# Kernel tuning notes

Measured on AMD Instinct MI355X. Metric: run time of the kernel, lower is better.

Reference implementation:

```python
import math
import jax, jax.numpy as jnp
import numpy as np

EPS = 1e-8


def setup_inputs() -> dict:
    key = jax.random.key(0)
    k0, k1, k2, k3 = jax.random.split(key, 4)
    B, C_IN, C_OUT, H, W, K, S = 8, 256, 256, 128, 128, 3, 512
    return {
        "input": jax.random.normal(k0, (B, C_IN, H, W), dtype=jnp.float32),
        "style": jax.random.normal(k1, (B, S), dtype=jnp.float32),
        # learned params
        "weight": jax.random.normal(k2, (1, C_OUT, C_IN, K, K), dtype=jnp.float32),
        "mod_weight": jax.random.normal(k3, (C_IN, S), dtype=jnp.float32),
        "mod_bias": jnp.ones((C_IN,), dtype=jnp.float32),  # bias_init=1
    }


def reference(input, style, weight, mod_weight, mod_bias):
    B, C_in, H, W = input.shape
    _, C_out, _, K, _ = weight.shape
    S = mod_weight.shape[1]

    # EqualLinear modulation: F.linear(style, w * (1/sqrt(S))) + bias (lr_mul=1)
    lin_scale = 1.0 / math.sqrt(S)
    s = style @ (mod_weight.T * lin_scale) + mod_bias  # [B, C_in]

    # per-sample weight modulation
    conv_scale = 1.0 / math.sqrt(C_in * K * K)  # fan_in scale
    w = conv_scale * weight * s[:, None, :, None, None]  # [B, C_out, C_in, K, K]

    # demodulation
    demod = jax.lax.rsqrt(jnp.sum(w * w, axis=(2, 3, 4)) + EPS)  # [B, C_out]
    w = w * demod[:, :, None, None, None]

    # groups=batch conv2d with padding=k//2 (same spatial size)
    pad = K // 2

    def conv_one(x, wk):  # x: [C_in, H, W], wk: [C_out, C_in, K, K]
        y = jax.lax.conv_general_dilated(
            x[None], wk, window_strides=(1, 1),
            padding=[(pad, pad), (pad, pad)],
            dimension_numbers=("NCHW", "OIHW", "NCHW"))
        return y[0]

    return jax.vmap(conv_one)(input, w)  # [B, C_out, H, W]
```

## Files before the change

### kernel.cpp

```cpp
#include <hip/hip_runtime.h>
#include <hip/hip_bf16.h>

typedef __attribute__((ext_vector_type(8))) short short8;
typedef __attribute__((ext_vector_type(4))) float floatx4;
typedef __attribute__((ext_vector_type(4))) unsigned uint4v;

#define B_ 8
#define C_IN 256
#define C_OUT 256
#define H_ 128
#define W_ 128
#define S_ 512
#define HW_ (H_*W_)
#define LIN_SCALE 0.04419417382415922f
#define CONV_SCALE 0.02083333333333333f
#define EPS_ 1e-8f

#define XPH 130
#define XPW 136
#define TTH 8
#define TTW 32
#define PH2 10
#define PW2 34
#define NPIX2 (PH2*PW2)
#define BUFSZ 24576
#define ABUFSZ 8192
#define ABASE_LDS 49152
#define NKB 72
#define NTHR 256

__device__ __forceinline__ unsigned short f2bf(float f) {
  unsigned u = __builtin_bit_cast(unsigned, f);
  u = (u + 0x7fffu + ((u >> 16) & 1u)) >> 16;
  return (unsigned short)u;
}
__device__ __forceinline__ unsigned pack2(float a, float b) {
  return (unsigned)f2bf(a) | ((unsigned)f2bf(b) << 16);
}
__device__ __forceinline__ void gload16(const void* g, void* l) {
  __builtin_amdgcn_global_load_lds(
      (const __attribute__((address_space(1))) unsigned*)g,
      (__attribute__((address_space(3))) unsigned*)l, 16, 0, 0);
}

__global__ void k_style(const float* __restrict__ style, const float* __restrict__ mw,
                        const float* __restrict__ mb, float* __restrict__ s) {
  __shared__ float sty[S_];
  const int b = blockIdx.x;
  for (int i = threadIdx.x; i < S_; i += 256) sty[i] = style[b*S_ + i];
  __syncthreads();
  const int ci = threadIdx.x;
  const float* wr = mw + (size_t)ci*S_;
  float acc = 0.f;
  for (int i = 0; i < S_; ++i) acc += sty[i] * wr[i];
  s[b*C_IN + ci] = acc * LIN_SCALE + mb[ci];
}

__global__ void k_demod(const float* __restrict__ weight, const float* __restrict__ s,
                        float* __restrict__ demod) {
  const int b = blockIdx.x >> 8, co = blockIdx.x & 255;
  const int l = threadIdx.x;
  const float* wrow = weight + (size_t)co*C_IN*9;
  const float* sb = s + b*C_IN;
  float acc = 0.f;
  for (int idx = l; idx < C_IN*9; idx += 64) {
    float wv = wrow[idx] * sb[idx/9];
    acc += wv*wv;
  }
#pragma unroll
  for (int off = 32; off; off >>= 1) acc += __shfl_down(acc, off, 64);
  if (l == 0) demod[blockIdx.x] = rsqrtf(acc * (CONV_SCALE*CONV_SCALE) + EPS_);
}

__global__ void k_pack(const float* __restrict__ weight, const float* __restrict__ s,
                       const float* __restrict__ demod, unsigned short* __restrict__ frag) {
  const int bid = blockIdx.x;
  const int mt = bid & 15;
  const int kb = (bid >> 4) % NKB;
  const int b  = bid / (NKB*16);
  const int l = threadIdx.x;
  const int co = mt*16 + (l & 15);
  const int chunk = kb / 9, r = kb % 9;
  const float dm = demod[b*C_OUT + co] * CONV_SCALE;
  const float* sb = s + b*C_IN;
  unsigned v[4];
#pragma unroll
  for (int jj = 0; jj < 4; ++jj) {
    int ci0 = chunk*32 + (l >> 4)*8 + jj*2;
    unsigned lo = f2bf(weight[((size_t)co*C_IN + ci0    )*9 + r] * sb[ci0    ] * dm);
    unsigned hi = f2bf(weight[((size_t)co*C_IN + ci0 + 1)*9 + r] * sb[ci0 + 1] * dm);
    v[jj] = lo | (hi << 16);
  }
  unsigned* dst = (unsigned*)(frag + (size_t)bid*512 + l*8);
  dst[0] = v[0]; dst[1] = v[1]; dst[2] = v[2]; dst[3] = v[3];
}

__global__ void k_border(unsigned short* __restrict__ xp) {
  const int plane = blockIdx.x;
  unsigned short* base = xp + (size_t)plane*XPH*XPW*32;
  const uint4v z = {0u,0u,0u,0u};
  for (int i = threadIdx.x; i < 516; i += 256) {
    int hh, ww;
    if (i < 260) { hh = (i < 130) ? 0 : 129; ww = i % 130; }
    else { int j = i - 260; ww = (j < 128) ? 0 : 129; hh = 1 + (j & 127); }
    uint4v* p = (uint4v*)(base + ((size_t)hh*XPW + ww)*32);
    p[0] = z; p[1] = z; p[2] = z; p[3] = z;
  }
}

__global__ void k_xpose(const float* __restrict__ x, unsigned short* __restrict__ xp) {
  __shared__ __align__(16) unsigned lds32[64*128];
  const int bid = blockIdx.x;
  const int half = bid & 1, h = (bid >> 1) & 127, b = bid >> 8;
  const int w0 = half*64;
  const int t = threadIdx.x;
  const float* xr = x + (size_t)b*C_IN*HW_ + (size_t)h*W_ + w0;
#pragma unroll
  for (int j = 0; j < 8; ++j) {
    int cp = j*16 + (t >> 4);
    int ci = cp*2;
    const float* p0 = xr + (size_t)ci*HW_ + (t & 15)*4;
    floatx4 f0 = *(const floatx4*)p0;
    floatx4 f1 = *(const floatx4*)(p0 + HW_);
    int g = cp >> 2, slot = cp & 3;
#pragma unroll
    for (int k = 0; k < 4; ++k) {
      int px = (t & 15)*4 + k;
      lds32[px*128 + ((g ^ ((px >> 2) & 7)) << 2) + slot] = pack2(f0[k], f1[k]);
    }
  }
  __syncthreads();
#pragma unroll
  for (int i = 0; i < 8; ++i) {
    int item = i*256 + t;
    int px = item >> 5, g = item & 31;
    int c = (item >> 2) & 7, sub = item & 3;
    int gs = g ^ ((px >> 2) & 7);
    uint4v v = *(const uint4v*)&lds32[px*128 + (gs << 2)];
    unsigned short* dst = xp +
        (((size_t)(b*8 + c)*XPH + (h + 1))*XPW + (w0 + 1 + px))*32 + sub*8;
    *(uint4v*)dst = v;
  }
}

__launch_bounds__(NTHR, 2)
__global__ void k_conv(const unsigned short* __restrict__ xpad,
                       const unsigned short* __restrict__ frag,
                       float* __restrict__ out) {
  __shared__ __align__(16) unsigned char sm[2*BUFSZ + 4*ABUFSZ];
  const int work = (blockIdx.x & 7)*128 + (blockIdx.x >> 3);
  const int ct = work & 1;
  const int w2 = work >> 1;
  const int sx = w2 & 3, sy = (w2 >> 2) & 15, b = w2 >> 6;
  const int h0 = sy*TTH, w0 = sx*TTW;
  const int tid = threadIdx.x;
  const int lane = tid & 63, wv = tid >> 6;
  const int wm = wv >> 1, wn = wv & 1;
  const int sl = lane >> 4, c15 = lane & 15, wn8 = wn*8;
  const int b8 = b*8;

  floatx4 acc[4][8];
#pragma unroll
  for (int m = 0; m < 4; ++m)
#pragma unroll
    for (int n = 0; n < 8; ++n) acc[m][n] = floatx4{0.f, 0.f, 0.f, 0.f};

  int srcoff[6];
#pragma unroll
  for (int p = 0; p < 6; ++p) {
    int item = p*256 + tid;
    int px = item >> 2, q8s = item & 3;
    if (px > NPIX2 - 1) px = NPIX2 - 1;
    int ph = px / PW2, pw = px - ph*PW2;
    int q8 = q8s ^ ((px >> 1) & 3);
    srcoff[p] = (ph*XPW + pw)*32 + q8*8;
  }
  const unsigned short* abase = frag + ((size_t)b*NKB*16 + ct*8)*512 + (size_t)tid*8;
  const unsigned char* aRd = sm + ABASE_LDS + wm*4096 + lane*16;

  short8 Ar[4], Br[8];

  auto readRegs = [&](int slot, int bbase, int tap) __attribute__((always_inline)) {
    const int dh = tap/3, dw = tap%3;
#pragma unroll
    for (int m = 0; m < 4; ++m)
      Ar[m] = *(const short8*)(aRd + slot*8192 + m*1024);
#pragma unroll
    for (int n = 0; n < 8; ++n) {
      int nt = wn8 + n;
      int pix = ((nt >> 1) + dh)*PW2 + ((nt & 1)*16 + c15 + dw);
      int addr = pix*64 + ((sl ^ ((pix >> 1) & 3)) << 4);
      Br[n] = *(const short8*)(sm + bbase + addr);
    }
  };
  auto mfmaStep = [&]() __attribute__((always_inline)) {
    __builtin_amdgcn_s_setprio(1);
#pragma unroll
    for (int n = 0; n < 8; ++n) {
      acc[0][n] = __builtin_amdgcn_mfma_f32_16x16x32_bf16(Ar[0], Br[n], acc[0][n], 0, 0, 0);
      acc[1][n] = __builtin_amdgcn_mfma_f32_16x16x32_bf16(Ar[1], Br[n], acc[1][n], 0, 0, 0);
      acc[2][n] = __builtin_amdgcn_mfma_f32_16x16x32_bf16(Ar[2], Br[n], acc[2][n], 0, 0, 0);
      acc[3][n] = __builtin_amdgcn_mfma_f32_16x16x32_bf16(Ar[3], Br[n], acc[3][n], 0, 0, 0);
    }
    __builtin_amdgcn_s_setprio(0);
  };

#define SBAR0 __builtin_amdgcn_sched_barrier(0)
#define WAITB(NLIT) do { SBAR0; \
    asm volatile("s_waitcnt vmcnt(" NLIT ")" ::: "memory"); \
    __builtin_amdgcn_s_barrier(); SBAR0; } while (0)

#define STEP(J, R, NLIT) do { \
    WAITB(NLIT); \
    { int kbs = c9 + (R) + 3; if (kbs > NKB-1) kbs = NKB-1; \
      const unsigned short* asrc = abase + (size_t)kbs*8192; \
      unsigned char* adst = sm + ABASE_LDS + ((((J)+(R)+3)&3)*8192) + tid*16; \
      gload16(asrc, adst); gload16(asrc + 2048, adst + 4096); } \
    if ((R) < 6) \
      gload16(xc + srcoff[R], sm + ((((J)+1)&1)*BUFSZ) + ((R)*256 + tid)*16); \
    mfmaStep(); \
    readRegs(((J)+(R)+1)&3, \
             ((R)==8) ? ((((J)+1)&1)*BUFSZ) : (((J)&1)*BUFSZ), \
             ((R)==8) ? 0 : (R)+1); \
  } while (0)

#define CHUNK(J) do { \
    const int c = cc*4 + (J); const int c9 = c*9; \
    const int cn = (c < 7) ? c + 1 : 7; \
    const unsigned short* xc = xpad + (((size_t)(b8 + cn)*XPH + h0)*XPW + w0)*32; \
    STEP(J,0,"2"); STEP(J,1,"3"); STEP(J,2,"3"); \
    STEP(J,3,"3"); STEP(J,4,"3"); STEP(J,5,"3"); \
    STEP(J,6,"3"); STEP(J,7,"2"); STEP(J,8,"2"); \
  } while (0)

  {
    const unsigned short* xc0 = xpad + (((size_t)b8*XPH + h0)*XPW + w0)*32;
#pragma unroll
    for (int p = 0; p < 6; ++p)
      gload16(xc0 + srcoff[p], sm + (p*256 + tid)*16);
#pragma unroll
    for (int s5 = 0; s5 < 3; ++s5) {
      const unsigned short* asrc = abase + (size_t)s5*8192;
      unsigned char* adst = sm + ABASE_LDS + s5*8192 + tid*16;
      gload16(asrc, adst); gload16(asrc + 2048, adst + 4096);
    }
    SBAR0;
    asm volatile("s_waitcnt vmcnt(0)" ::: "memory");
    __builtin_amdgcn_s_barrier();
    SBAR0;
    readRegs(0, 0, 0);
  }

#pragma unroll 1
  for (int cc = 0; cc < 2; ++cc) {
    CHUNK(0); CHUNK(1); CHUNK(2); CHUNK(3);
  }
#undef CHUNK
#undef STEP
#undef WAITB
#undef SBAR0

  float* ob = out + ((size_t)b*C_OUT + ct*128)*HW_;
  const int tw = lane & 15, rg = lane >> 4;
#pragma unroll
  for (int m = 0; m < 4; ++m) {
#pragma unroll
    for (int n = 0; n < 8; ++n) {
      int co = (wm*4 + m)*16 + rg*4;
      int nt = wn8 + n;
      int h = h0 + (nt >> 1);
      int w = w0 + (nt & 1)*16 + tw;
      float* p = ob + (size_t)co*HW_ + (size_t)h*W_ + w;
#pragma unroll
      for (int i = 0; i < 4; ++i) p[i*HW_] = acc[m][n][i];
    }
  }
}

extern "C" void kernel_launch(void* const* d_in, const int* in_sizes, int n_in,
                              void* d_out, int out_size, void* d_ws, size_t ws_size,
                              hipStream_t stream) {
  const float* x      = (const float*)d_in[0];
  const float* style  = (const float*)d_in[1];
  const float* weight = (const float*)d_in[2];
  const float* mod_w  = (const float*)d_in[3];
  const float* mod_b  = (const float*)d_in[4];
  float* out = (float*)d_out;
  char* ws = (char*)d_ws;

  float* s     = (float*)ws;
  float* demod = (float*)(ws + 8192);
  unsigned short* frag = (unsigned short*)(ws + 16384);
  unsigned short* xpad = (unsigned short*)(ws + (16u<<20));

  k_style<<<B_, 256, 0, stream>>>(style, mod_w, mod_b, s);
  k_demod<<<B_*C_OUT, 64, 0, stream>>>(weight, s, demod);
  k_pack<<<B_*NKB*16, 64, 0, stream>>>(weight, s, demod, frag);
  k_border<<<B_*8, 256, 0, stream>>>(xpad);
  k_xpose<<<B_*H_*2, 256, 0, stream>>>(x, xpad);
  k_conv<<<B_*2*16*4, NTHR, 0, stream>>>(xpad, frag, out);
}
```

Measured before the change: 211.6 us.

## Fuse border zeroing into transpose, batch k_pack taps, relax conv vmcnt waits

k_pack now handles all nine kernel taps per block, reading each contiguous 9-float weight row once instead of doing strided per-tap loads, and it launches a ninth as many blocks. The separate k_border launch is removed: k_xpose now zeroes the left/right padding columns for its row and the top/bottom rows when h==0. The vmcnt wait counts in the conv pipeline are loosened from 3 to 4 for the middle steps, allowing more loads in flight. This is meant to cut launch overhead and weight-packing traffic, and to overlap more memory latency in the conv. It risks a hazard if the looser waits let an MFMA read LDS data that has not arrived yet.

```diff
diff --git a/kernel.cpp b/kernel.cpp
--- a/kernel.cpp
+++ b/kernel.cpp
@@ -76,35 +76,29 @@
                        const float* __restrict__ demod, unsigned short* __restrict__ frag) {
   const int bid = blockIdx.x;
   const int mt = bid & 15;
-  const int kb = (bid >> 4) % NKB;
-  const int b  = bid / (NKB*16);
+  const int chunk = (bid >> 4) & 7;
+  const int b  = bid >> 7;
   const int l = threadIdx.x;
   const int co = mt*16 + (l & 15);
-  const int chunk = kb / 9, r = kb % 9;
   const float dm = demod[b*C_OUT + co] * CONV_SCALE;
   const float* sb = s + b*C_IN;
-  unsigned v[4];
+  unsigned v[9][4];
 #pragma unroll
   for (int jj = 0; jj < 4; ++jj) {
     int ci0 = chunk*32 + (l >> 4)*8 + jj*2;
-    unsigned lo = f2bf(weight[((size_t)co*C_IN + ci0    )*9 + r] * sb[ci0    ] * dm);
-    unsigned hi = f2bf(weight[((size_t)co*C_IN + ci0 + 1)*9 + r] * sb[ci0 + 1] * dm);
-    v[jj] = lo | (hi << 16);
-  }
-  unsigned* dst = (unsigned*)(frag + (size_t)bid*512 + l*8);
-  dst[0] = v[0]; dst[1] = v[1]; dst[2] = v[2]; dst[3] = v[3];
-}
-
-__global__ void k_border(unsigned short* __restrict__ xp) {
-  const int plane = blockIdx.x;
-  unsigned short* base = xp + (size_t)plane*XPH*XPW*32;
-  const uint4v z = {0u,0u,0u,0u};
-  for (int i = threadIdx.x; i < 516; i += 256) {
-    int hh, ww;
-    if (i < 260) { hh = (i < 130) ? 0 : 129; ww = i % 130; }
-    else { int j = i - 260; ww = (j < 128) ? 0 : 129; hh = 1 + (j & 127); }
-    uint4v* p = (uint4v*)(base + ((size_t)hh*XPW + ww)*32);
-    p[0] = z; p[1] = z; p[2] = z; p[3] = z;
+    float w0[9], w1[9];
+    __builtin_memcpy(w0, weight + ((size_t)co*C_IN + ci0    )*9, 36);
+    __builtin_memcpy(w1, weight + ((size_t)co*C_IN + ci0 + 1)*9, 36);
+    float s0 = sb[ci0] * dm, s1 = sb[ci0 + 1] * dm;
+#pragma unroll
+    for (int r = 0; r < 9; ++r)
+      v[r][jj] = pack2(w0[r]*s0, w1[r]*s1);
+  }
+#pragma unroll
+  for (int r = 0; r < 9; ++r) {
+    unsigned* dst = (unsigned*)(frag +
+        ((size_t)((b*NKB + chunk*9 + r)*16 + mt))*512 + l*8);
+    dst[0] = v[r][0]; dst[1] = v[r][1]; dst[2] = v[r][2]; dst[3] = v[r][3];
   }
 }
 
@@ -114,6 +108,23 @@
   const int half = bid & 1, h = (bid >> 1) & 127, b = bid >> 8;
   const int w0 = half*64;
   const int t = threadIdx.x;
+  const uint4v z = {0u,0u,0u,0u};
+  if (t < 32) {
+    int chunk = t >> 2, part = t & 3;
+    unsigned short* p = xp +
+        (((size_t)(b*8 + chunk)*XPH + (h + 1))*XPW + half*129)*32 + part*8;
+    *(uint4v*)p = z;
+  }
+  if (h == 0) {
+    for (int i = t; i < 65*2*8*4; i += 256) {
+      int part = i & 3, cell = i >> 2;
+      int wwi = cell % 65; int rest = cell / 65;
+      int rowsel = rest & 1, chunk = rest >> 1;
+      unsigned short* p = xp +
+          (((size_t)(b*8 + chunk)*XPH + rowsel*129)*XPW + (half*65 + wwi))*32 + part*8;
+      *(uint4v*)p = z;
+    }
+  }
   const float* xr = x + (size_t)b*C_IN*HW_ + (size_t)h*W_ + w0;
 #pragma unroll
   for (int j = 0; j < 8; ++j) {
@@ -228,9 +239,9 @@
     const int c = cc*4 + (J); const int c9 = c*9; \
     const int cn = (c < 7) ? c + 1 : 7; \
     const unsigned short* xc = xpad + (((size_t)(b8 + cn)*XPH + h0)*XPW + w0)*32; \
-    STEP(J,0,"2"); STEP(J,1,"3"); STEP(J,2,"3"); \
-    STEP(J,3,"3"); STEP(J,4,"3"); STEP(J,5,"3"); \
-    STEP(J,6,"3"); STEP(J,7,"2"); STEP(J,8,"2"); \
+    STEP(J,0,"2"); STEP(J,1,"3"); STEP(J,2,"4"); \
+    STEP(J,3,"4"); STEP(J,4,"4"); STEP(J,5,"4"); \
+    STEP(J,6,"4"); STEP(J,7,"3"); STEP(J,8,"2"); \
   } while (0)
 
   {
@@ -295,8 +306,7 @@
 
   k_style<<<B_, 256, 0, stream>>>(style, mod_w, mod_b, s);
   k_demod<<<B_*C_OUT, 64, 0, stream>>>(weight, s, demod);
-  k_pack<<<B_*NKB*16, 64, 0, stream>>>(weight, s, demod, frag);
-  k_border<<<B_*8, 256, 0, stream>>>(xpad);
+  k_pack<<<B_*8*16, 64, 0, stream>>>(weight, s, demod, frag);
   k_xpose<<<B_*H_*2, 256, 0, stream>>>(x, xpad);
   k_conv<<<B_*2*16*4, NTHR, 0, stream>>>(xpad, frag, out);
 }
```

Result: faster. 201.0 us (-5.0%).
